# Kernel tuning notes

Hardware: AMD Instinct MI355X
Metric: run time of the kernel (lower is better)

The kernel has to match this reference:

```python
import jax, jax.numpy as jnp
import numpy as np

D_HEAD = 64  # module's self.heads scaling constant


def setup_inputs() -> dict:
    key = jax.random.key(0)
    kq, kk, kv = jax.random.split(key, 3)
    N, HW, C = 4, 4096, 64
    Q = jax.random.normal(kq, (N, HW, C), dtype=jnp.float32)
    K = jax.random.normal(kk, (N, HW, C), dtype=jnp.float32)
    V = jax.random.normal(kv, (N, HW, C), dtype=jnp.float32)
    return {"Q": Q, "K": K, "V": V}


def reference(Q, K, V):
    # logits[n, q, k] = Q[n,q,:] . K[n,k,:] / sqrt(d_head)
    scale = 1.0 / jnp.sqrt(jnp.asarray(D_HEAD, dtype=Q.dtype))
    logits = jnp.einsum("nqc,nkc->nqk", Q, K) * scale  # [N, HW, HW]
    # NOTE: softmax over the QUERY axis (dim=1), non-standard
    attn = jax.nn.softmax(logits, axis=1)
    return jnp.einsum("nqk,nkc->nqc", attn, V)
```

## Files before the change

### kernel.cpp

```cpp
#include <hip/hip_runtime.h>
#include <hip/hip_bf16.h>

#define NB 4
#define HWN 4096
#define CD 64
#define NSTRIDE (HWN * CD)

typedef short short8 __attribute__((ext_vector_type(8), may_alias));
typedef short short4v __attribute__((ext_vector_type(4), may_alias));
typedef float f32x4 __attribute__((ext_vector_type(4), may_alias));
typedef unsigned int uint4v __attribute__((ext_vector_type(4), may_alias));

__device__ constexpr float C1 = 0.18033688011112042f;

__device__ __forceinline__ unsigned short f2bf(float f) {
    unsigned u = __builtin_bit_cast(unsigned, f);
    u = (u + 0x7FFFu + ((u >> 16) & 1u)) >> 16;
    return (unsigned short)u;
}

__device__ __forceinline__ float fexp2(float x) {
#if __has_builtin(__builtin_amdgcn_exp2f)
    return __builtin_amdgcn_exp2f(x);
#else
    return exp2f(x);
#endif
}

__device__ __forceinline__ unsigned pk2(float a, float b) {
    __hip_bfloat162 h = __float22bfloat162_rn(float2{a, b});
    unsigned u;
    __builtin_memcpy(&u, &h, 4);
    return u;
}

__device__ __forceinline__ size_t qk_swz(int row, int c) {
    return (size_t)(row >> 4) * 1024 + (c >> 5) * 512 +
           ((((c >> 3) & 3) * 16 + (row & 15)) * 8) + (c & 7);
}

__device__ __forceinline__ int k_perm_row(int r) {
    int G = r >> 5, a = r & 31;
    int j = a & 7, g = a >> 3;
    return (G << 5) + ((j >> 2) << 4) + g * 4 + (j & 3);
}

__global__ __launch_bounds__(256) void cvt_qk(const float* __restrict__ Q,
                                              const float* __restrict__ K,
                                              unsigned short* __restrict__ Qs,
                                              unsigned short* __restrict__ Ks,
                                              float* __restrict__ l) {
    if (blockIdx.x < 16) {
        int zi = blockIdx.x * 256 + threadIdx.x;
        *(f32x4*)(l + (size_t)zi * 4) = f32x4{0.f, 0.f, 0.f, 0.f};
    }
    int i = (blockIdx.x * 256 + threadIdx.x) * 4;
    int rg = i >> 6, c = i & 63;
    int n = rg >> 12, r = rg & 4095;
    float4 q = *(const float4*)(Q + i);
    float4 k = *(const float4*)(K + i);
    ushort4 qo, ko;
    qo.x = f2bf(q.x * C1); qo.y = f2bf(q.y * C1);
    qo.z = f2bf(q.z * C1); qo.w = f2bf(q.w * C1);
    ko.x = f2bf(k.x); ko.y = f2bf(k.y); ko.z = f2bf(k.z); ko.w = f2bf(k.w);
    *(ushort4*)(Qs + (size_t)n * NSTRIDE + qk_swz(r, c)) = qo;
    *(ushort4*)(Ks + (size_t)n * NSTRIDE + qk_swz(k_perm_row(r), c)) = ko;
}

__global__ __attribute__((amdgpu_flat_work_group_size(256, 256), amdgpu_waves_per_eu(2, 4)))
void lsum_kernel(const unsigned short* __restrict__ Qs,
                 const unsigned short* __restrict__ Ks,
                 float* __restrict__ l) {
    int tid = threadIdx.x;
    int w = tid >> 6, lane = tid & 63, quad = lane >> 4, m16 = lane & 15;
    int n = blockIdx.y;
    int kbase = blockIdx.x * 256 + w * 64;

    const unsigned short* Kp = Ks + (size_t)n * NSTRIDE + (kbase >> 4) * 1024 + lane * 8;
    short8 ka0 = *(const short8*)(Kp);
    short8 ka1 = *(const short8*)(Kp + 512);
    short8 kb0 = *(const short8*)(Kp + 1024);
    short8 kb1 = *(const short8*)(Kp + 1536);
    short8 kc0 = *(const short8*)(Kp + 2048);
    short8 kc1 = *(const short8*)(Kp + 2560);
    short8 kd0 = *(const short8*)(Kp + 3072);
    short8 kd1 = *(const short8*)(Kp + 3584);

    const unsigned short* Qp = Qs + (size_t)n * NSTRIDE + blockIdx.z * 16384 + lane * 8;

    short8 qc0 = *(const short8*)(Qp);
    short8 qc1 = *(const short8*)(Qp + 512);
    Qp += 1024;

    float lA[4] = {0.f, 0.f, 0.f, 0.f};
    float lB[4] = {0.f, 0.f, 0.f, 0.f};
    float lC[4] = {0.f, 0.f, 0.f, 0.f};
    float lD[4] = {0.f, 0.f, 0.f, 0.f};
#pragma unroll 2
    for (int qc = 0; qc < 16; ++qc) {
        short8 qn0 = *(const short8*)(Qp);
        short8 qn1 = *(const short8*)(Qp + 512);
        f32x4 a = {0.f, 0.f, 0.f, 0.f}, b = a, c = a, d = a;
        __builtin_amdgcn_s_setprio(1);
        a = __builtin_amdgcn_mfma_f32_16x16x32_bf16(ka0, qc0, a, 0, 0, 0);
        a = __builtin_amdgcn_mfma_f32_16x16x32_bf16(ka1, qc1, a, 0, 0, 0);
        b = __builtin_amdgcn_mfma_f32_16x16x32_bf16(kb0, qc0, b, 0, 0, 0);
        b = __builtin_amdgcn_mfma_f32_16x16x32_bf16(kb1, qc1, b, 0, 0, 0);
        c = __builtin_amdgcn_mfma_f32_16x16x32_bf16(kc0, qc0, c, 0, 0, 0);
        c = __builtin_amdgcn_mfma_f32_16x16x32_bf16(kc1, qc1, c, 0, 0, 0);
        d = __builtin_amdgcn_mfma_f32_16x16x32_bf16(kd0, qc0, d, 0, 0, 0);
        d = __builtin_amdgcn_mfma_f32_16x16x32_bf16(kd1, qc1, d, 0, 0, 0);
        __builtin_amdgcn_s_setprio(0);
#pragma unroll
        for (int r = 0; r < 4; ++r) {
            lA[r] += fexp2(a[r]);
            lB[r] += fexp2(b[r]);
            lC[r] += fexp2(c[r]);
            lD[r] += fexp2(d[r]);
        }
        qc0 = qn0; qc1 = qn1;
        Qp += 1024;
    }
#pragma unroll
    for (int r = 0; r < 4; ++r)
        for (int d1 = 1; d1 < 16; d1 <<= 1) {
            lA[r] += __shfl_xor(lA[r], d1);
            lB[r] += __shfl_xor(lB[r], d1);
            lC[r] += __shfl_xor(lC[r], d1);
            lD[r] += __shfl_xor(lD[r], d1);
        }
    if (m16 == 0) {
        float* lp = l + n * HWN + kbase + quad * 8;
#pragma unroll
        for (int r = 0; r < 4; ++r) {
            atomicAdd(lp + r, lA[r]);
            atomicAdd(lp + 4 + r, lB[r]);
            atomicAdd(lp + 32 + r, lC[r]);
            atomicAdd(lp + 36 + r, lD[r]);
        }
    }
}

__global__ __launch_bounds__(256) void prep_v(const float* __restrict__ V,
                                              const float* __restrict__ l,
                                              unsigned short* __restrict__ Vts) {
    __shared__ float rl[64];
    __shared__ float tile[64][65];
    int tid = threadIdx.x, n = blockIdx.y, kbase = blockIdx.x * 64;
    if (tid < 64) rl[tid] = 1.0f / l[n * HWN + kbase + tid];
    __syncthreads();
#pragma unroll
    for (int i = 0; i < 16; ++i) {
        int e = i * 256 + tid;
        int k = e >> 6, c = e & 63;
        tile[c][k] = V[((size_t)(n * HWN + kbase + k)) * CD + c] * rl[k];
    }
    __syncthreads();
#pragma unroll
    for (int i = 0; i < 2; ++i) {
        int s = i * 256 + tid;
        int kb32 = s >> 8;
        int ct = (s >> 6) & 3;
        int ll = s & 63;
        int cc = ct * 16 + (ll & 15);
        int k0 = kb32 * 32 + ((ll >> 4) & 3) * 8;
        short8 v;
#pragma unroll
        for (int j = 0; j < 8; ++j)
            v[j] = (short)f2bf(tile[cc][k0 + j]);
        size_t off = (size_t)n * NSTRIDE + (size_t)((kbase >> 5) + kb32) * 2048 +
                     ct * 512 + ll * 8;
        *(short8*)(Vts + off) = v;
    }
}

__global__ __attribute__((amdgpu_flat_work_group_size(256, 256), amdgpu_waves_per_eu(2, 4)))
void attn_kernel(const unsigned short* __restrict__ Qs,
                 const unsigned short* __restrict__ Ks,
                 const unsigned short* __restrict__ Vts,
                 float* __restrict__ partial,
                 int nit) {
    int tid = threadIdx.x;
    int w = tid >> 6, lane = tid & 63, quad = lane >> 4, m16 = lane & 15;
    int n = blockIdx.y;
    int qbase = blockIdx.x * 128 + w * 16;

    const unsigned short* Qp = Qs + (size_t)n * NSTRIDE + (qbase >> 4) * 1024 + lane * 8;
    short8 qa0 = *(const short8*)(Qp);
    short8 qa1 = *(const short8*)(Qp + 512);
    short8 qb0 = *(const short8*)(Qp + 4096);
    short8 qb1 = *(const short8*)(Qp + 4096 + 512);

    size_t kofs = (size_t)blockIdx.z * (size_t)nit * 2048;
    const unsigned short* Kp = Ks + (size_t)n * NSTRIDE + kofs + lane * 8;
    const unsigned short* Vp = Vts + (size_t)n * NSTRIDE + kofs + lane * 8;

    f32x4 oA[4], oB[4];
#pragma unroll
    for (int ct = 0; ct < 4; ++ct) { oA[ct] = f32x4{0.f, 0.f, 0.f, 0.f}; oB[ct] = oA[ct]; }

    short8 kf00 = *(const short8*)(Kp);
    short8 kf01 = *(const short8*)(Kp + 512);
    short8 kf10 = *(const short8*)(Kp + 1024);
    short8 kf11 = *(const short8*)(Kp + 1536);

#pragma unroll 2
    for (int it = 0; it < nit; ++it) {
        short8 kn00 = *(const short8*)(Kp + 2048);
        short8 kn01 = *(const short8*)(Kp + 2560);
        short8 kn10 = *(const short8*)(Kp + 3072);
        short8 kn11 = *(const short8*)(Kp + 3584);
        short8 vf0 = *(const short8*)(Vp);
        short8 vf1 = *(const short8*)(Vp + 512);
        short8 vf2 = *(const short8*)(Vp + 1024);
        short8 vf3 = *(const short8*)(Vp + 1536);

        f32x4 s00 = {0.f, 0.f, 0.f, 0.f}, s01 = s00, s10 = s00, s11 = s00;
        __builtin_amdgcn_s_setprio(1);
        s00 = __builtin_amdgcn_mfma_f32_16x16x32_bf16(kf00, qa0, s00, 0, 0, 0);
        s00 = __builtin_amdgcn_mfma_f32_16x16x32_bf16(kf01, qa1, s00, 0, 0, 0);
        s01 = __builtin_amdgcn_mfma_f32_16x16x32_bf16(kf10, qa0, s01, 0, 0, 0);
        s01 = __builtin_amdgcn_mfma_f32_16x16x32_bf16(kf11, qa1, s01, 0, 0, 0);
        s10 = __builtin_amdgcn_mfma_f32_16x16x32_bf16(kf00, qb0, s10, 0, 0, 0);
        s10 = __builtin_amdgcn_mfma_f32_16x16x32_bf16(kf01, qb1, s10, 0, 0, 0);
        s11 = __builtin_amdgcn_mfma_f32_16x16x32_bf16(kf10, qb0, s11, 0, 0, 0);
        s11 = __builtin_amdgcn_mfma_f32_16x16x32_bf16(kf11, qb1, s11, 0, 0, 0);
        __builtin_amdgcn_s_setprio(0);

        uint4v wa = {pk2(fexp2(s00[0]), fexp2(s00[1])), pk2(fexp2(s00[2]), fexp2(s00[3])),
                     pk2(fexp2(s01[0]), fexp2(s01[1])), pk2(fexp2(s01[2]), fexp2(s01[3]))};
        uint4v wb = {pk2(fexp2(s10[0]), fexp2(s10[1])), pk2(fexp2(s10[2]), fexp2(s10[3])),
                     pk2(fexp2(s11[0]), fexp2(s11[1])), pk2(fexp2(s11[2]), fexp2(s11[3]))};
        short8 pA = __builtin_bit_cast(short8, wa);
        short8 pB = __builtin_bit_cast(short8, wb);

        __builtin_amdgcn_s_setprio(1);
        oA[0] = __builtin_amdgcn_mfma_f32_16x16x32_bf16(vf0, pA, oA[0], 0, 0, 0);
        oB[0] = __builtin_amdgcn_mfma_f32_16x16x32_bf16(vf0, pB, oB[0], 0, 0, 0);
        oA[1] = __builtin_amdgcn_mfma_f32_16x16x32_bf16(vf1, pA, oA[1], 0, 0, 0);
        oB[1] = __builtin_amdgcn_mfma_f32_16x16x32_bf16(vf1, pB, oB[1], 0, 0, 0);
        oA[2] = __builtin_amdgcn_mfma_f32_16x16x32_bf16(vf2, pA, oA[2], 0, 0, 0);
        oB[2] = __builtin_amdgcn_mfma_f32_16x16x32_bf16(vf2, pB, oB[2], 0, 0, 0);
        oA[3] = __builtin_amdgcn_mfma_f32_16x16x32_bf16(vf3, pA, oA[3], 0, 0, 0);
        oB[3] = __builtin_amdgcn_mfma_f32_16x16x32_bf16(vf3, pB, oB[3], 0, 0, 0);
        __builtin_amdgcn_s_setprio(0);

        kf00 = kn00; kf01 = kn01; kf10 = kn10; kf11 = kn11;
        Kp += 2048;
        Vp += 2048;
    }

    float* ppA = partial + (size_t)blockIdx.z * (NB * HWN * CD) +
                 ((size_t)(n * HWN + qbase + m16)) * CD + quad * 4;
    float* ppB = ppA + (size_t)64 * CD;
#pragma unroll
    for (int ct = 0; ct < 4; ++ct) {
        *(f32x4*)(ppA + ct * 16) = oA[ct];
        *(f32x4*)(ppB + ct * 16) = oB[ct];
    }
}

__global__ __launch_bounds__(256) void reduce_out(const float* __restrict__ p,
                                                  float* __restrict__ out, int ns) {
    int i = (blockIdx.x * 256 + threadIdx.x) * 4;
    f32x4 a = *(const f32x4*)(p + i);
    for (int s = 1; s < ns; ++s)
        a = a + *(const f32x4*)(p + (size_t)s * (NB * HWN * CD) + i);
    *(f32x4*)(out + i) = a;
}

extern "C" void kernel_launch(void* const* d_in, const int* in_sizes, int n_in,
                              void* d_out, int out_size, void* d_ws, size_t ws_size,
                              hipStream_t stream) {
    const float* Q = (const float*)d_in[0];
    const float* K = (const float*)d_in[1];
    const float* V = (const float*)d_in[2];
    float* out = (float*)d_out;

    char* ws = (char*)d_ws;
    unsigned short* Qs  = (unsigned short*)(ws);
    unsigned short* Ks  = (unsigned short*)(ws + (1u << 21));
    unsigned short* Vts = (unsigned short*)(ws + (2u << 21));
    float* l       = (float*)(ws + (3u << 21));
    float* partial = (float*)(ws + (4u << 21));

    size_t base = (size_t)(4u << 21);
    size_t slice = (size_t)NB * HWN * CD * sizeof(float);
    int ns = (ws_size >= base + 8 * slice) ? 8
           : (ws_size >= base + 4 * slice) ? 4 : 2;
    int nit = HWN / ns / 32;

    cvt_qk<<<1024, 256, 0, stream>>>(Q, K, Qs, Ks, l);
    lsum_kernel<<<dim3(16, NB, 16), 256, 0, stream>>>(Qs, Ks, l);
    prep_v<<<dim3(64, NB), 256, 0, stream>>>(V, l, Vts);
    attn_kernel<<<dim3(32, NB, ns), 256, 0, stream>>>(Qs, Ks, Vts, partial, nit);
    reduce_out<<<1024, 256, 0, stream>>>(partial, out, ns);
}
```

Baseline: 112.1 us.

## Fold V transpose into convert kernel and apply 1/l inside attention loop

The separate prep_v kernel is removed. The V transpose and bf16 conversion move into the Q/K conversion kernel, done by blocks 256-511. The per-key normalisation 1/l is no longer folded into V; the attention kernel loads the reciprocals for its key span into shared memory and multiplies them into the exponentiated probabilities before packing to bf16. This saves one kernel launch and a dependency stage, at the cost of extra multiplies and LDS reads in the hot loop plus a block-wide sync.

```diff
diff --git a/kernel.cpp b/kernel.cpp
--- a/kernel.cpp
+++ b/kernel.cpp
@@ -45,26 +45,59 @@
     return (G << 5) + ((j >> 2) << 4) + g * 4 + (j & 3);
 }
 
-__global__ __launch_bounds__(256) void cvt_qk(const float* __restrict__ Q,
-                                              const float* __restrict__ K,
-                                              unsigned short* __restrict__ Qs,
-                                              unsigned short* __restrict__ Ks,
-                                              float* __restrict__ l) {
+__global__ __launch_bounds__(256) void cvt_qkv(const float* __restrict__ Q,
+                                               const float* __restrict__ K,
+                                               const float* __restrict__ V,
+                                               unsigned short* __restrict__ Qs,
+                                               unsigned short* __restrict__ Ks,
+                                               unsigned short* __restrict__ Vts,
+                                               float* __restrict__ l) {
+    __shared__ float tile[64][65];
+    int tid = threadIdx.x;
     if (blockIdx.x < 16) {
-        int zi = blockIdx.x * 256 + threadIdx.x;
+        int zi = blockIdx.x * 256 + tid;
         *(f32x4*)(l + (size_t)zi * 4) = f32x4{0.f, 0.f, 0.f, 0.f};
     }
-    int i = (blockIdx.x * 256 + threadIdx.x) * 4;
-    int rg = i >> 6, c = i & 63;
-    int n = rg >> 12, r = rg & 4095;
-    float4 q = *(const float4*)(Q + i);
-    float4 k = *(const float4*)(K + i);
-    ushort4 qo, ko;
-    qo.x = f2bf(q.x * C1); qo.y = f2bf(q.y * C1);
-    qo.z = f2bf(q.z * C1); qo.w = f2bf(q.w * C1);
-    ko.x = f2bf(k.x); ko.y = f2bf(k.y); ko.z = f2bf(k.z); ko.w = f2bf(k.w);
-    *(ushort4*)(Qs + (size_t)n * NSTRIDE + qk_swz(r, c)) = qo;
-    *(ushort4*)(Ks + (size_t)n * NSTRIDE + qk_swz(k_perm_row(r), c)) = ko;
+    {
+        int i = (blockIdx.x * 256 + tid) * 4;
+        int rg = i >> 6, c = i & 63;
+        int n = rg >> 12, r = rg & 4095;
+        float4 q = *(const float4*)(Q + i);
+        float4 k = *(const float4*)(K + i);
+        ushort4 qo, ko;
+        qo.x = f2bf(q.x * C1); qo.y = f2bf(q.y * C1);
+        qo.z = f2bf(q.z * C1); qo.w = f2bf(q.w * C1);
+        ko.x = f2bf(k.x); ko.y = f2bf(k.y); ko.z = f2bf(k.z); ko.w = f2bf(k.w);
+        *(ushort4*)(Qs + (size_t)n * NSTRIDE + qk_swz(r, c)) = qo;
+        *(ushort4*)(Ks + (size_t)n * NSTRIDE + qk_swz(k_perm_row(r), c)) = ko;
+    }
+    if (blockIdx.x >= 256 && blockIdx.x < 512) {
+        int bx = blockIdx.x - 256;
+        int n = bx >> 6, kbase = (bx & 63) * 64;
+#pragma unroll
+        for (int i = 0; i < 16; ++i) {
+            int e = i * 256 + tid;
+            int k = e >> 6, c = e & 63;
+            tile[c][k] = V[((size_t)(n * HWN + kbase + k)) * CD + c];
+        }
+        __syncthreads();
+#pragma unroll
+        for (int i = 0; i < 2; ++i) {
+            int s = i * 256 + tid;
+            int kb32 = s >> 8;
+            int ct = (s >> 6) & 3;
+            int ll = s & 63;
+            int cc = ct * 16 + (ll & 15);
+            int k0 = kb32 * 32 + ((ll >> 4) & 3) * 8;
+            short8 v;
+#pragma unroll
+            for (int j = 0; j < 8; ++j)
+                v[j] = (short)f2bf(tile[cc][k0 + j]);
+            size_t off = (size_t)n * NSTRIDE + (size_t)((kbase >> 5) + kb32) * 2048 +
+                         ct * 512 + ll * 8;
+            *(short8*)(Vts + off) = v;
+        }
+    }
 }
 
 __global__ __attribute__((amdgpu_flat_work_group_size(256, 256), amdgpu_waves_per_eu(2, 4)))
@@ -141,49 +174,23 @@
     }
 }
 
-__global__ __launch_bounds__(256) void prep_v(const float* __restrict__ V,
-                                              const float* __restrict__ l,
-                                              unsigned short* __restrict__ Vts) {
-    __shared__ float rl[64];
-    __shared__ float tile[64][65];
-    int tid = threadIdx.x, n = blockIdx.y, kbase = blockIdx.x * 64;
-    if (tid < 64) rl[tid] = 1.0f / l[n * HWN + kbase + tid];
-    __syncthreads();
-#pragma unroll
-    for (int i = 0; i < 16; ++i) {
-        int e = i * 256 + tid;
-        int k = e >> 6, c = e & 63;
-        tile[c][k] = V[((size_t)(n * HWN + kbase + k)) * CD + c] * rl[k];
-    }
-    __syncthreads();
-#pragma unroll
-    for (int i = 0; i < 2; ++i) {
-        int s = i * 256 + tid;
-        int kb32 = s >> 8;
-        int ct = (s >> 6) & 3;
-        int ll = s & 63;
-        int cc = ct * 16 + (ll & 15);
-        int k0 = kb32 * 32 + ((ll >> 4) & 3) * 8;
-        short8 v;
-#pragma unroll
-        for (int j = 0; j < 8; ++j)
-            v[j] = (short)f2bf(tile[cc][k0 + j]);
-        size_t off = (size_t)n * NSTRIDE + (size_t)((kbase >> 5) + kb32) * 2048 +
-                     ct * 512 + ll * 8;
-        *(short8*)(Vts + off) = v;
-    }
-}
-
 __global__ __attribute__((amdgpu_flat_work_group_size(256, 256), amdgpu_waves_per_eu(2, 4)))
 void attn_kernel(const unsigned short* __restrict__ Qs,
                  const unsigned short* __restrict__ Ks,
                  const unsigned short* __restrict__ Vts,
+                 const float* __restrict__ l,
                  float* __restrict__ partial,
                  int nit) {
+    __shared__ float rls[2048];
     int tid = threadIdx.x;
     int w = tid >> 6, lane = tid & 63, quad = lane >> 4, m16 = lane & 15;
     int n = blockIdx.y;
     int qbase = blockIdx.x * 128 + w * 16;
+
+    int kspan = nit * 32;
+    int kk0 = blockIdx.z * kspan;
+    for (int i = tid; i < kspan; i += 256)
+        rls[i] = 1.0f / l[n * HWN + kk0 + i];
 
     const unsigned short* Qp = Qs + (size_t)n * NSTRIDE + (qbase >> 4) * 1024 + lane * 8;
     short8 qa0 = *(const short8*)(Qp);
@@ -203,6 +210,8 @@
     short8 kf01 = *(const short8*)(Kp + 512);
     short8 kf10 = *(const short8*)(Kp + 1024);
     short8 kf11 = *(const short8*)(Kp + 1536);
+
+    __syncthreads();
 
 #pragma unroll 2
     for (int it = 0; it < nit; ++it) {
@@ -227,10 +236,18 @@
         s11 = __builtin_amdgcn_mfma_f32_16x16x32_bf16(kf11, qb1, s11, 0, 0, 0);
         __builtin_amdgcn_s_setprio(0);
 
-        uint4v wa = {pk2(fexp2(s00[0]), fexp2(s00[1])), pk2(fexp2(s00[2]), fexp2(s00[3])),
-                     pk2(fexp2(s01[0]), fexp2(s01[1])), pk2(fexp2(s01[2]), fexp2(s01[3]))};
-        uint4v wb = {pk2(fexp2(s10[0]), fexp2(s10[1])), pk2(fexp2(s10[2]), fexp2(s10[3])),
-                     pk2(fexp2(s11[0]), fexp2(s11[1])), pk2(fexp2(s11[2]), fexp2(s11[3]))};
+        const float* rlp = rls + it * 32 + quad * 8;
+        f32x4 rlo = *(const f32x4*)(rlp);
+        f32x4 rhi = *(const f32x4*)(rlp + 4);
+
+        uint4v wa = {pk2(fexp2(s00[0]) * rlo[0], fexp2(s00[1]) * rlo[1]),
+                     pk2(fexp2(s00[2]) * rlo[2], fexp2(s00[3]) * rlo[3]),
+                     pk2(fexp2(s01[0]) * rhi[0], fexp2(s01[1]) * rhi[1]),
+                     pk2(fexp2(s01[2]) * rhi[2], fexp2(s01[3]) * rhi[3])};
+        uint4v wb = {pk2(fexp2(s10[0]) * rlo[0], fexp2(s10[1]) * rlo[1]),
+                     pk2(fexp2(s10[2]) * rlo[2], fexp2(s10[3]) * rlo[3]),
+                     pk2(fexp2(s11[0]) * rhi[0], fexp2(s11[1]) * rhi[1]),
+                     pk2(fexp2(s11[2]) * rhi[2], fexp2(s11[3]) * rhi[3])};
         short8 pA = __builtin_bit_cast(short8, wa);
         short8 pB = __builtin_bit_cast(short8, wb);
 
@@ -290,9 +307,8 @@
            : (ws_size >= base + 4 * slice) ? 4 : 2;
     int nit = HWN / ns / 32;
 
-    cvt_qk<<<1024, 256, 0, stream>>>(Q, K, Qs, Ks, l);
+    cvt_qkv<<<1024, 256, 0, stream>>>(Q, K, V, Qs, Ks, Vts, l);
     lsum_kernel<<<dim3(16, NB, 16), 256, 0, stream>>>(Qs, Ks, l);
-    prep_v<<<dim3(64, NB), 256, 0, stream>>>(V, l, Vts);
-    attn_kernel<<<dim3(32, NB, ns), 256, 0, stream>>>(Qs, Ks, Vts, partial, nit);
+    attn_kernel<<<dim3(32, NB, ns), 256, 0, stream>>>(Qs, Ks, Vts, l, partial, nit);
     reduce_out<<<1024, 256, 0, stream>>>(partial, out, ns);
 }
```

Measured after the change: 112.3 us. No clear change (+0.1%).
